# Optimization experiments

Hardware: AMD Instinct MI355X
Metric: run time of the kernel (lower is better)

## Reference

```python
import jax, jax.numpy as jnp
import numpy as np
import math

ALGEBRA_DIM = 32

def _hadamard(n):
    H = np.array([[1.0]], dtype=np.float32)
    while H.shape[0] < n:
        H = np.block([[H, H], [H, -H]])
    return H

# Sylvester-ordered Hadamard matrix, normalized: equals the butterfly FHT with /sqrt(N)
H32 = jnp.asarray(_hadamard(ALGEBRA_DIM) / math.sqrt(ALGEBRA_DIM), dtype=jnp.float32)

def quantize_ternary(w):
    # BitNet-b1.58 style absmean ternary quantization with straight-through estimator
    scale = jnp.mean(jnp.abs(w)) + 1e-8
    w_q = jnp.clip(jnp.round(w / scale), -1.0, 1.0) * scale
    return w + jax.lax.stop_gradient(w_q - w)

def setup_inputs() -> dict:
    key = jax.random.key(0)
    k1, k2, k3 = jax.random.split(key, 3)
    B, T = 4, 2048
    in_o = out_o = 128  # in_features = out_features = 4096
    x = jax.random.normal(k1, (B, T, ALGEBRA_DIM * in_o), dtype=jnp.float32)
    weight = jax.random.uniform(k2, (ALGEBRA_DIM, out_o, in_o), dtype=jnp.float32) * 2.0 - 1.0
    alpha = jnp.ones((ALGEBRA_DIM, in_o), dtype=jnp.float32)
    beta_init = math.sqrt(3.0 / (2.0 * in_o))
    beta = jnp.ones((ALGEBRA_DIM, out_o), dtype=jnp.float32) * beta_init
    return {"x": x, "weight": weight, "alpha": alpha, "beta": beta}

def reference(x, weight, alpha, beta):
    B, T, D = x.shape
    G = ALGEBRA_DIM
    in_o = D // G
    w_q = quantize_ternary(weight)                      # [G, out_o, in_o]
    xp = x.reshape(B, T, G, in_o) * alpha               # [B,T,G,in_o]
    # FHT over algebra dim G (Sylvester WHT, /sqrt(G) folded into H32)
    xm = jnp.einsum('btgi,gh->bthi', xp, H32)           # [B,T,G,in_o]
    # grouped ternary matmul: btgi,gio->btgo with w_q transposed
    yp = jnp.einsum('bthi,hoi->btho', xm, w_q)          # [B,T,G,out_o]
    ym = jnp.einsum('btho,hg->btgo', yp, H32)           # FHT over algebra dim again
    y = ym * beta                                       # [B,T,G,out_o]
    return y.reshape(B, T, -1)
```

## Files before the change

kernel.cpp:

```cpp
#include <hip/hip_runtime.h>
#include <cstdint>
#include <cstddef>

#define TM 8
#define IP 136
#define SLAB (TM * IP)

__device__ __forceinline__ unsigned short f2bf(float f) {
  union { float f; unsigned int u; } c; c.f = f;
  unsigned int u = c.u;
  return (unsigned short)((u + 0x7FFFu + ((u >> 16) & 1u)) >> 16);
}
__device__ __forceinline__ float bf2f(unsigned short h) {
  union { unsigned int u; float f; } c; c.u = ((unsigned int)h) << 16; return c.f;
}

__device__ __forceinline__ void fht32(float* v) {
  #pragma unroll
  for (int s = 1; s < 32; s <<= 1) {
    #pragma unroll
    for (int a = 0; a < 32; ++a) {
      if ((a & s) == 0) {
        float u0 = v[a], u1 = v[a + s];
        v[a] = u0 + u1;
        v[a + s] = u0 - u1;
      }
    }
  }
}

typedef __attribute__((ext_vector_type(8))) short bf16x8;
typedef __attribute__((ext_vector_type(4))) float f32x4;

__global__ void kred1(const float* __restrict__ w, double* __restrict__ partials) {
  const int tid = threadIdx.x;
  const int base = blockIdx.x * 2048 + tid;
  double s = 0.0;
  #pragma unroll
  for (int j = 0; j < 8; ++j) s += (double)fabsf(w[base + j * 256]);
  #pragma unroll
  for (int off = 32; off > 0; off >>= 1) s += __shfl_down(s, off, 64);
  __shared__ double sh[4];
  if ((tid & 63) == 0) sh[tid >> 6] = s;
  __syncthreads();
  if (tid == 0) partials[blockIdx.x] = sh[0] + sh[1] + sh[2] + sh[3];
}

__global__ void kprep(const float* __restrict__ w, const double* __restrict__ partials,
                      float* __restrict__ scale_out, unsigned short* __restrict__ wqt) {
  const int tid = threadIdx.x;
  __shared__ float s_sc;
  if (tid < 64) {
    double s = partials[tid] + partials[tid + 64] + partials[tid + 128] + partials[tid + 192];
    #pragma unroll
    for (int off = 32; off > 0; off >>= 1) s += __shfl_down(s, off, 64);
    if (tid == 0) s_sc = (float)(s / 524288.0) + 1e-8f;
  }
  __syncthreads();
  const float sc = s_sc;
  if (blockIdx.x == 0 && tid == 0) scale_out[0] = sc;
  const int cid = blockIdx.x * 256 + tid;
  const int lane = cid & 63, ks = (cid >> 6) & 3, nt = (cid >> 8) & 7, h = cid >> 11;
  const int m = lane & 15, quad = lane >> 4;
  const float* src = w + h * 16384 + (nt * 16 + m) * 128 + ks * 32 + quad * 8;
  bf16x8 vv;
  #pragma unroll
  for (int j = 0; j < 8; ++j) {
    float q = rintf(src[j] / sc);
    q = fminf(1.f, fmaxf(-1.f, q));
    vv[j] = (short)f2bf(q);
  }
  *(bf16x8*)(wqt + (size_t)cid * 8) = vv;
}

__global__ __launch_bounds__(512, 4) void had_main(
    const float* __restrict__ x,
    const unsigned short* __restrict__ wqt,
    const float* __restrict__ alpha,
    const float* __restrict__ beta,
    const float* __restrict__ scale_p,
    float* __restrict__ y) {
  extern __shared__ unsigned short lds[];
  const int tid = threadIdx.x;
  const long tok0 = (long)blockIdx.x * TM;
  const int i0 = tid & 127;
  const int tq = tid >> 7;

  {
    const float* xrowA = x + (size_t)(tok0 + tq) * 4096 + i0;
    const float* xrowB = x + (size_t)(tok0 + tq + 4) * 4096 + i0;
    float va[32], vb[32];
    #pragma unroll
    for (int g = 0; g < 32; ++g) va[g] = xrowA[(size_t)g * 128];
    #pragma unroll
    for (int g = 0; g < 32; ++g) vb[g] = xrowB[(size_t)g * 128];
    #pragma unroll
    for (int g = 0; g < 32; ++g) {
      const float a = alpha[g * 128 + i0];
      va[g] *= a; vb[g] *= a;
    }
    fht32(va);
    #pragma unroll
    for (int h = 0; h < 32; ++h) lds[(h * TM + tq) * IP + i0] = f2bf(va[h]);
    fht32(vb);
    #pragma unroll
    for (int h = 0; h < 32; ++h) lds[(h * TM + tq + 4) * IP + i0] = f2bf(vb[h]);
  }
  __syncthreads();

  {
    const int wave = tid >> 6;
    const int lane = tid & 63;
    const int m = lane & 15;
    const int quad = lane >> 4;
    #pragma unroll
    for (int hh = 0; hh < 4; ++hh) {
      const int h = wave + hh * 8;
      unsigned short* slab = lds + h * SLAB;
      bf16x8 afr[4];
      #pragma unroll
      for (int ks = 0; ks < 4; ++ks)
        afr[ks] = *(const bf16x8*)(slab + (m & 7) * IP + ks * 32 + quad * 8);
      const unsigned short* wh = wqt + (size_t)h * 16384 + (size_t)lane * 8;
      bf16x8 cur[4], nxt[4];
      #pragma unroll
      for (int ks = 0; ks < 4; ++ks) cur[ks] = *(const bf16x8*)(wh + ks * 512);
      #pragma unroll
      for (int nt = 0; nt < 8; ++nt) {
        if (nt < 7) {
          #pragma unroll
          for (int ks = 0; ks < 4; ++ks)
            nxt[ks] = *(const bf16x8*)(wh + (size_t)((nt + 1) * 4 + ks) * 512);
        }
        f32x4 acc = {0.f, 0.f, 0.f, 0.f};
        #pragma unroll
        for (int ks = 0; ks < 4; ++ks)
          acc = __builtin_amdgcn_mfma_f32_16x16x32_bf16(afr[ks], cur[ks], acc, 0, 0, 0);
        if (quad < 2) {
          #pragma unroll
          for (int r = 0; r < 4; ++r)
            slab[(quad * 4 + r) * IP + nt * 16 + m] = f2bf(acc[r]);
        }
        #pragma unroll
        for (int ks = 0; ks < 4; ++ks) cur[ks] = nxt[ks];
      }
    }
  }
  __syncthreads();

  {
    const float sc32 = scale_p[0] * (1.0f / 32.0f);
    float cf[32];
    #pragma unroll
    for (int g = 0; g < 32; ++g) cf[g] = beta[g * 128 + i0] * sc32;
    #pragma unroll
    for (int p = 0; p < 2; ++p) {
      const int t = tq + p * 4;
      float v[32];
      #pragma unroll
      for (int h = 0; h < 32; ++h) v[h] = bf2f(lds[(h * TM + t) * IP + i0]);
      fht32(v);
      float* yrow = y + (size_t)(tok0 + t) * 4096 + i0;
      #pragma unroll
      for (int g = 0; g < 32; ++g) yrow[(size_t)g * 128] = v[g] * cf[g];
    }
  }
}

extern "C" void kernel_launch(void* const* d_in, const int* in_sizes, int n_in,
                              void* d_out, int out_size, void* d_ws, size_t ws_size,
                              hipStream_t stream) {
  (void)in_sizes; (void)n_in; (void)out_size; (void)ws_size;
  const float* x     = (const float*)d_in[0];
  const float* w     = (const float*)d_in[1];
  const float* alpha = (const float*)d_in[2];
  const float* beta  = (const float*)d_in[3];
  float* y = (float*)d_out;

  char* ws = (char*)d_ws;
  unsigned short* wqt = (unsigned short*)(ws);
  float* scale     = (float*)(ws + 1048576);
  double* partials = (double*)(ws + 1048584);

  (void)hipFuncSetAttribute(reinterpret_cast<const void*>(had_main),
                            hipFuncAttributeMaxDynamicSharedMemorySize, 69632);

  hipLaunchKernelGGL(kred1,    dim3(256),  dim3(256), 0,     stream, w, partials);
  hipLaunchKernelGGL(kprep,    dim3(256),  dim3(256), 0,     stream, w, partials, scale, wqt);
  hipLaunchKernelGGL(had_main, dim3(1024), dim3(512), 69632, stream, x, wqt, alpha, beta, scale, y);
}
```

Baseline: 273.3 us.

## Process 16 tokens per block to fill MFMA tiles and vectorize I/O

Doubles the tokens per block from 8 to 16, so each 16x16 MFMA tile uses all 16 rows instead of discarding half, and each weight fragment load is reused across twice as many tokens. Blocks grow to 1024 threads with 136 KB of LDS, and each thread now handles two adjacent input columns with float2 global loads and stores and packed bf16 LDS writes. The weight fetch moves to a three-deep rolling register prefetch across two h-slabs per wave. The cost is larger LDS per block and higher register pressure, which could reduce occupancy to one block per CU.

Result: no change. 272.4 us (-0.3%).

```diff
diff --git a/kernel.cpp b/kernel.cpp
--- a/kernel.cpp
+++ b/kernel.cpp
@@ -2,7 +2,7 @@
 #include <cstdint>
 #include <cstddef>
 
-#define TM 8
+#define TM 16
 #define IP 136
 #define SLAB (TM * IP)
 
@@ -31,6 +31,7 @@
 
 typedef __attribute__((ext_vector_type(8))) short bf16x8;
 typedef __attribute__((ext_vector_type(4))) float f32x4;
+typedef __attribute__((ext_vector_type(2))) float f32x2;
 
 __global__ void kred1(const float* __restrict__ w, double* __restrict__ partials) {
   const int tid = threadIdx.x;
@@ -73,7 +74,7 @@
   *(bf16x8*)(wqt + (size_t)cid * 8) = vv;
 }
 
-__global__ __launch_bounds__(512, 4) void had_main(
+__global__ __launch_bounds__(1024, 4) void had_main(
     const float* __restrict__ x,
     const unsigned short* __restrict__ wqt,
     const float* __restrict__ alpha,
@@ -83,28 +84,29 @@
   extern __shared__ unsigned short lds[];
   const int tid = threadIdx.x;
   const long tok0 = (long)blockIdx.x * TM;
-  const int i0 = tid & 127;
-  const int tq = tid >> 7;
+  const int t  = tid >> 6;
+  const int ih = (tid & 63) << 1;
 
   {
-    const float* xrowA = x + (size_t)(tok0 + tq) * 4096 + i0;
-    const float* xrowB = x + (size_t)(tok0 + tq + 4) * 4096 + i0;
+    const float* xrow = x + (size_t)(tok0 + t) * 4096 + ih;
     float va[32], vb[32];
     #pragma unroll
-    for (int g = 0; g < 32; ++g) va[g] = xrowA[(size_t)g * 128];
-    #pragma unroll
-    for (int g = 0; g < 32; ++g) vb[g] = xrowB[(size_t)g * 128];
-    #pragma unroll
     for (int g = 0; g < 32; ++g) {
-      const float a = alpha[g * 128 + i0];
-      va[g] *= a; vb[g] *= a;
+      f32x2 v = *(const f32x2*)(xrow + (size_t)g * 128);
+      va[g] = v[0]; vb[g] = v[1];
+    }
+    #pragma unroll
+    for (int g = 0; g < 32; ++g) {
+      f32x2 a = *(const f32x2*)(alpha + g * 128 + ih);
+      va[g] *= a[0]; vb[g] *= a[1];
     }
     fht32(va);
-    #pragma unroll
-    for (int h = 0; h < 32; ++h) lds[(h * TM + tq) * IP + i0] = f2bf(va[h]);
     fht32(vb);
     #pragma unroll
-    for (int h = 0; h < 32; ++h) lds[(h * TM + tq + 4) * IP + i0] = f2bf(vb[h]);
+    for (int h = 0; h < 32; ++h) {
+      unsigned int pk = (unsigned int)f2bf(va[h]) | ((unsigned int)f2bf(vb[h]) << 16);
+      *(unsigned int*)(lds + (h * TM + t) * IP + ih) = pk;
+    }
   }
   __syncthreads();
 
@@ -113,56 +115,65 @@
     const int lane = tid & 63;
     const int m = lane & 15;
     const int quad = lane >> 4;
-    #pragma unroll
-    for (int hh = 0; hh < 4; ++hh) {
-      const int h = wave + hh * 8;
-      unsigned short* slab = lds + h * SLAB;
-      bf16x8 afr[4];
+    unsigned short* slab0 = lds + (wave)      * SLAB;
+    unsigned short* slab1 = lds + (wave + 16) * SLAB;
+    bf16x8 af0[4], af1[4];
+    #pragma unroll
+    for (int ks = 0; ks < 4; ++ks) {
+      af0[ks] = *(const bf16x8*)(slab0 + m * IP + ks * 32 + quad * 8);
+      af1[ks] = *(const bf16x8*)(slab1 + m * IP + ks * 32 + quad * 8);
+    }
+    const unsigned short* wh0 = wqt + (size_t)(wave)      * 16384 + (size_t)lane * 8;
+    const unsigned short* wh1 = wqt + (size_t)(wave + 16) * 16384 + (size_t)lane * 8;
+    bf16x8 b0[4], b1[4], b2[4];
+    #pragma unroll
+    for (int ks = 0; ks < 4; ++ks) b0[ks] = *(const bf16x8*)(wh0 + (size_t)ks * 512);
+    #pragma unroll
+    for (int ks = 0; ks < 4; ++ks) b1[ks] = *(const bf16x8*)(wh0 + (size_t)(4 + ks) * 512);
+    #pragma unroll
+    for (int s = 0; s < 16; ++s) {
+      const int nt = s & 7;
+      if (s < 14) {
+        const int s2 = s + 2;
+        const unsigned short* wsrc =
+            (s2 < 8 ? wh0 : wh1) + (size_t)((s2 & 7) * 4) * 512;
+        #pragma unroll
+        for (int ks = 0; ks < 4; ++ks) b2[ks] = *(const bf16x8*)(wsrc + (size_t)ks * 512);
+      }
+      f32x4 acc = {0.f, 0.f, 0.f, 0.f};
+      const bf16x8* af = (s < 8) ? af0 : af1;
       #pragma unroll
       for (int ks = 0; ks < 4; ++ks)
-        afr[ks] = *(const bf16x8*)(slab + (m & 7) * IP + ks * 32 + quad * 8);
-      const unsigned short* wh = wqt + (size_t)h * 16384 + (size_t)lane * 8;
-      bf16x8 cur[4], nxt[4];
+        acc = __builtin_amdgcn_mfma_f32_16x16x32_bf16(af[ks], b0[ks], acc, 0, 0, 0);
+      unsigned short* slab = (s < 8) ? slab0 : slab1;
       #pragma unroll
-      for (int ks = 0; ks < 4; ++ks) cur[ks] = *(const bf16x8*)(wh + ks * 512);
+      for (int r = 0; r < 4; ++r)
+        slab[(quad * 4 + r) * IP + nt * 16 + m] = f2bf(acc[r]);
       #pragma unroll
-      for (int nt = 0; nt < 8; ++nt) {
-        if (nt < 7) {
-          #pragma unroll
-          for (int ks = 0; ks < 4; ++ks)
-            nxt[ks] = *(const bf16x8*)(wh + (size_t)((nt + 1) * 4 + ks) * 512);
-        }
-        f32x4 acc = {0.f, 0.f, 0.f, 0.f};
-        #pragma unroll
-        for (int ks = 0; ks < 4; ++ks)
-          acc = __builtin_amdgcn_mfma_f32_16x16x32_bf16(afr[ks], cur[ks], acc, 0, 0, 0);
-        if (quad < 2) {
-          #pragma unroll
-          for (int r = 0; r < 4; ++r)
-            slab[(quad * 4 + r) * IP + nt * 16 + m] = f2bf(acc[r]);
-        }
-        #pragma unroll
-        for (int ks = 0; ks < 4; ++ks) cur[ks] = nxt[ks];
-      }
+      for (int ks = 0; ks < 4; ++ks) { b0[ks] = b1[ks]; b1[ks] = b2[ks]; }
     }
   }
   __syncthreads();
 
   {
     const float sc32 = scale_p[0] * (1.0f / 32.0f);
-    float cf[32];
-    #pragma unroll
-    for (int g = 0; g < 32; ++g) cf[g] = beta[g * 128 + i0] * sc32;
-    #pragma unroll
-    for (int p = 0; p < 2; ++p) {
-      const int t = tq + p * 4;
-      float v[32];
-      #pragma unroll
-      for (int h = 0; h < 32; ++h) v[h] = bf2f(lds[(h * TM + t) * IP + i0]);
-      fht32(v);
-      float* yrow = y + (size_t)(tok0 + t) * 4096 + i0;
-      #pragma unroll
-      for (int g = 0; g < 32; ++g) yrow[(size_t)g * 128] = v[g] * cf[g];
+    float v0[32], v1[32];
+    #pragma unroll
+    for (int h = 0; h < 32; ++h) {
+      unsigned int pk = *(const unsigned int*)(lds + (h * TM + t) * IP + ih);
+      v0[h] = bf2f((unsigned short)(pk & 0xFFFFu));
+      v1[h] = bf2f((unsigned short)(pk >> 16));
+    }
+    fht32(v0);
+    fht32(v1);
+    float* yrow = y + (size_t)(tok0 + t) * 4096 + ih;
+    #pragma unroll
+    for (int g = 0; g < 32; ++g) {
+      f32x2 b = *(const f32x2*)(beta + g * 128 + ih);
+      const float c0 = b[0] * sc32;
+      const float c1 = b[1] * sc32;
+      f32x2 o; o[0] = v0[g] * c0; o[1] = v1[g] * c1;
+      *(f32x2*)(yrow + (size_t)g * 128) = o;
     }
   }
 }
@@ -183,9 +194,9 @@
   double* partials = (double*)(ws + 1048584);
 
   (void)hipFuncSetAttribute(reinterpret_cast<const void*>(had_main),
-                            hipFuncAttributeMaxDynamicSharedMemorySize, 69632);
-
-  hipLaunchKernelGGL(kred1,    dim3(256),  dim3(256), 0,     stream, w, partials);
-  hipLaunchKernelGGL(kprep,    dim3(256),  dim3(256), 0,     stream, w, partials, scale, wqt);
-  hipLaunchKernelGGL(had_main, dim3(1024), dim3(512), 69632, stream, x, wqt, alpha, beta, scale, y);
-}
+                            hipFuncAttributeMaxDynamicSharedMemorySize, 139264);
+
+  hipLaunchKernelGGL(kred1,    dim3(256), dim3(256),  0,      stream, w, partials);
+  hipLaunchKernelGGL(kprep,    dim3(256), dim3(256),  0,      stream, w, partials, scale, wqt);
+  hipLaunchKernelGGL(had_main, dim3(512), dim3(1024), 139264, stream, x, wqt, alpha, beta, scale, y);
+}
```
